# Optimization experiments

Measured on AMD Instinct MI355X. Metric: run time of the kernel, lower is better.

Reference implementation:

```python
import jax, jax.numpy as jnp
import numpy as np
from jax import lax

K = 16        # patch_size / kernel_size
S = 16        # stride
EMB = 768     # embed_dim
CIN = 3


def setup_inputs() -> dict:
    key = jax.random.key(0)
    k1, k2, k3, k4, k5 = jax.random.split(key, 5)
    B, H, W = 64, 384, 384
    pixel_values = jax.random.normal(k1, (B, CIN, H, W), jnp.float32)
    # offset conv: Conv2d(3, 2*K*K, kernel=K, stride=K); small init so offsets stay moderate
    offset_w = jax.random.normal(k2, (2 * K * K, CIN, K, K), jnp.float32) * 0.01
    offset_b = jax.random.normal(k3, (2 * K * K,), jnp.float32) * 0.01
    # deformable projection: DeformConv2d(3, 768, kernel=K, stride=K)
    proj_w = jax.random.normal(k4, (EMB, CIN, K, K), jnp.float32) * 0.02
    proj_b = jax.random.normal(k5, (EMB,), jnp.float32) * 0.02
    return {"pixel_values": pixel_values, "offset_w": offset_w, "offset_b": offset_b,
            "proj_w": proj_w, "proj_b": proj_b}


def _bilinear_gather(img, py, px):
    """img: [B,C,H,W]; py,px: [B,K,K,HO,WO] float sample coords.
    Returns [B,C,K,K,HO,WO] with zero padding outside the image (torchvision semantics)."""
    B, C, H, W = img.shape
    shp = py.shape
    y0 = jnp.floor(py); x0 = jnp.floor(px)
    wy1 = py - y0; wy0 = 1.0 - wy1
    wx1 = px - x0; wx0 = 1.0 - wx1
    imgf = img.reshape(B, C, H * W)

    def corner(yy, xx, w):
        valid = (yy >= 0) & (yy < H) & (xx >= 0) & (xx < W)
        yi = jnp.clip(yy, 0, H - 1).astype(jnp.int32)
        xi = jnp.clip(xx, 0, W - 1).astype(jnp.int32)
        idx = (yi * W + xi).reshape(B, -1)                       # [B, N]
        v = jnp.take_along_axis(imgf, idx[:, None, :], axis=2)   # [B, C, N]
        return v * (jnp.where(valid, w, 0.0)).reshape(B, 1, -1)

    val = (corner(y0, x0, wy0 * wx0) + corner(y0, x0 + 1, wy0 * wx1)
           + corner(y0 + 1, x0, wy1 * wx0) + corner(y0 + 1, x0 + 1, wy1 * wx1))
    return val.reshape((B, C) + shp[1:])


def reference(pixel_values, offset_w, offset_b, proj_w, proj_b):
    B, C, H, W = pixel_values.shape
    HO, WO = H // S, W // S
    # offset conv (dense, stride=patch, VALID padding)
    offset = lax.conv_general_dilated(pixel_values, offset_w, (S, S), 'VALID',
                                      dimension_numbers=('NCHW', 'OIHW', 'NCHW'))
    offset = offset + offset_b[None, :, None, None]              # [B, 2*K*K, HO, WO]
    off = offset.reshape(B, K * K, 2, HO, WO)
    dy = off[:, :, 0].reshape(B, K, K, HO, WO)
    dx = off[:, :, 1].reshape(B, K, K, HO, WO)
    # base sampling grid: p = (ho*S + i + dy, wo*S + j + dx)
    base_y = (jnp.arange(HO, dtype=jnp.float32) * S)[None, None, None, :, None] \
             + jnp.arange(K, dtype=jnp.float32)[None, :, None, None, None]
    base_x = (jnp.arange(WO, dtype=jnp.float32) * S)[None, None, None, None, :] \
             + jnp.arange(K, dtype=jnp.float32)[None, None, :, None, None]
    py = base_y + dy
    px = base_x + dx
    sampled = _bilinear_gather(pixel_values, py, px)             # [B, C, K, K, HO, WO]
    out = jnp.einsum('bcijhw,ocij->bohw', sampled, proj_w) + proj_b[None, :, None, None]
    # flatten(2).transpose(1,2) -> [B, HO*WO, EMB]
    return out.reshape(B, EMB, HO * WO).transpose(0, 2, 1)
```

## Files before the change

kernel.cpp:

```cpp
#include <hip/hip_runtime.h>
#include <stdint.h>

typedef __bf16 bf16x8 __attribute__((ext_vector_type(8)));
typedef float  f32x4  __attribute__((ext_vector_type(4)));

#define HH 384
#define WW 384
#define NPIX (HH*WW)
#define NC 3
#define NPATCH 576
#define EMB 768
#define PLEN 768
#define MLOC 32
#define KSTEPS 24
#define NLOC (64*576)
#define NTILES (NLOC/MLOC)
#define NT1 4
#define W1_UNITS (32*KSTEPS*64)
#define W2_UNITS (48*KSTEPS*64)
#define W2_OFF   (W1_UNITS*8)
#define SA_OFF   ((W1_UNITS+W2_UNITS)*8)
#define WBLKS  ((W1_UNITS + W2_UNITS) / 256)

__device__ __forceinline__ uint16_t f2bf(float f) {
    uint32_t u = __builtin_bit_cast(uint32_t, f);
    u += 0x7FFFu + ((u >> 16) & 1u);
    return (uint16_t)(u >> 16);
}
__device__ __forceinline__ uint32_t pk2(float a, float b) {
    return (uint32_t)f2bf(a) | ((uint32_t)f2bf(b) << 16);
}
__device__ __forceinline__ float bf2f(uint16_t u) {
    return __builtin_bit_cast(float, (uint32_t)u << 16);
}

__global__ __launch_bounds__(256)
void prepass_w(const float* __restrict__ offw, const float* __restrict__ projw,
               uint16_t* __restrict__ wz) {
    int u = blockIdx.x * 256 + threadIdx.x;
    const float* src;
    int uu;
    if (u < W1_UNITS) { src = offw; uu = u; }
    else              { src = projw; uu = u - W1_UNITS; }
    int lane = uu & 63;
    int t    = uu >> 6;
    int ks   = t % KSTEPS;
    int nt   = t / KSTEPS;
    int n    = nt * 16 + (lane & 15);
    int k0   = ks * 32 + (lane >> 4) * 8;
    const float4* s4 = (const float4*)(src + (size_t)n * PLEN + k0);
    float4 v0 = s4[0], v1 = s4[1];
    uint4 w;
    w.x = pk2(v0.x, v0.y); w.y = pk2(v0.z, v0.w);
    w.z = pk2(v1.x, v1.y); w.w = pk2(v1.z, v1.w);
    *(uint4*)(wz + (size_t)u * 8) = w;
}

__global__ __launch_bounds__(512, 4)
void k1_offsets(const float* __restrict__ pix,
                const float* __restrict__ offb,
                const uint16_t* __restrict__ wz,
                uint16_t* __restrict__ sa) {
    __shared__ __align__(16) uint16_t As[MLOC][PLEN];

    const int tid  = threadIdx.x;
    const int wv   = tid >> 6;
    const int lane = tid & 63;
    const int lr   = lane & 15;
    const int lg   = lane >> 4;
    const int sw0  = (lr & 7) << 3;
    const int even = ((lane & 1) == 0);

    int bid = (int)blockIdx.x;
    const int tile = (bid & 7) * 144 + (bid >> 3);
    const int loc0 = tile * MLOC;
    const int bimg = loc0 / NPATCH;
    const int p0   = loc0 - bimg * NPATCH;
    const float* __restrict__ pb = pix + (size_t)bimg * NC * NPIX;

    #pragma unroll
    for (int uu = 0; uu < 6; ++uu) {
        int unit = tid + uu * 512;
        int loc  = unit / 96;
        int k8   = (unit - loc * 96) * 8;
        int c  = k8 >> 8;
        int i  = (k8 >> 4) & 15;
        int j  = k8 & 15;
        int p  = p0 + loc;
        int ho = p / 24;
        int wo = p - ho * 24;
        const float* g = pb + ((size_t)c * HH + ho * 16 + i) * WW + wo * 16 + j;
        float4 v0 = *(const float4*)g;
        float4 v1 = *(const float4*)(g + 4);
        uint4 w;
        w.x = pk2(v0.x, v0.y); w.y = pk2(v0.z, v0.w);
        w.z = pk2(v1.x, v1.y); w.w = pk2(v1.z, v1.w);
        *(uint4*)&As[loc][k8 ^ ((loc & 7) << 3)] = w;
    }

    auto ldb1 = [&](int ntg, int ks) -> bf16x8 {
        return *(const bf16x8*)(wz + ((size_t)((ntg * KSTEPS + ks) * 64 + lane)) * 8);
    };
    bf16x8 b1a[NT1], b1b[NT1];
    #pragma unroll
    for (int nt = 0; nt < NT1; ++nt) b1a[nt] = ldb1(wv * NT1 + nt, 0);
    __syncthreads();

    f32x4 acc1[2][NT1];
    #pragma unroll
    for (int nt = 0; nt < NT1; ++nt) {
        float bz = offb[(wv * NT1 + nt) * 16 + lr];
        f32x4 z = {bz, bz, bz, bz};
        acc1[0][nt] = z; acc1[1][nt] = z;
    }
    #pragma unroll 1
    for (int ks2 = 0; ks2 < KSTEPS / 2; ++ks2) {
        const int ks0 = ks2 * 2;
        {
            #pragma unroll
            for (int nt = 0; nt < NT1; ++nt) b1b[nt] = ldb1(wv * NT1 + nt, ks0 + 1);
            int ke = (ks0 * 32 + lg * 8) ^ sw0;
            bf16x8 a0 = *(const bf16x8*)&As[lr][ke];
            bf16x8 a1 = *(const bf16x8*)&As[16 + lr][ke];
            #pragma unroll
            for (int nt = 0; nt < NT1; ++nt) {
                acc1[0][nt] = __builtin_amdgcn_mfma_f32_16x16x32_bf16(a0, b1a[nt], acc1[0][nt], 0, 0, 0);
                acc1[1][nt] = __builtin_amdgcn_mfma_f32_16x16x32_bf16(a1, b1a[nt], acc1[1][nt], 0, 0, 0);
            }
        }
        {
            int ksn = (ks0 + 2 < KSTEPS) ? ks0 + 2 : 0;
            #pragma unroll
            for (int nt = 0; nt < NT1; ++nt) b1a[nt] = ldb1(wv * NT1 + nt, ksn);
            int ke = ((ks0 + 1) * 32 + lg * 8) ^ sw0;
            bf16x8 a0 = *(const bf16x8*)&As[lr][ke];
            bf16x8 a1 = *(const bf16x8*)&As[16 + lr][ke];
            #pragma unroll
            for (int nt = 0; nt < NT1; ++nt) {
                acc1[0][nt] = __builtin_amdgcn_mfma_f32_16x16x32_bf16(a0, b1b[nt], acc1[0][nt], 0, 0, 0);
                acc1[1][nt] = __builtin_amdgcn_mfma_f32_16x16x32_bf16(a1, b1b[nt], acc1[1][nt], 0, 0, 0);
            }
        }
    }

    #pragma unroll
    for (int nt = 0; nt < NT1; ++nt)
      #pragma unroll
      for (int mt = 0; mt < 2; ++mt)
        #pragma unroll
        for (int r = 0; r < 4; ++r) {
            float v  = acc1[mt][nt][r];
            float pv = __shfl_xor(v, 1);
            if ((nt < 2) == (even != 0)) {
                int s   = nt & 1;
                int loc = mt * 16 + lg * 4 + r;
                int q   = (wv * NT1 + (even ? 0 : 2) + s) * 8 + (lr >> 1);
                float dy = even ? v  : pv;
                float dx = even ? pv : v;
                ((uint32_t*)(sa + (size_t)(loc0 + loc) * PLEN))[q] = pk2(dy, dx);
            }
        }
}

__global__ __launch_bounds__(512)
void k2_gather(const float* __restrict__ pix, uint16_t* __restrict__ sa) {
    const int tid  = threadIdx.x;
    const int wv   = tid >> 6;
    const int lane = tid & 63;

    int bid = (int)blockIdx.x;
    const int tile = (bid & 7) * 144 + (bid >> 3);
    const int loc0 = tile * MLOC;
    const int bimg = loc0 / NPATCH;
    const int p0   = loc0 - bimg * NPATCH;
    const float* __restrict__ pb = pix + (size_t)bimg * NC * NPIX;

    #pragma unroll
    for (int li = 0; li < 4; ++li) {
        const int L   = wv * 4 + li;
        const int p   = p0 + L;
        const int ho  = p / 24;
        const int wo  = p - ho * 24;
        const int by  = ho * 16;
        const int bx  = wo * 16;
        uint16_t* row = sa + (size_t)(loc0 + L) * PLEN;
        const uint32_t* rowu = (const uint32_t*)row;
        uint32_t od0 = rowu[       lane];
        uint32_t od1 = rowu[ 64 +  lane];
        uint32_t od2 = rowu[128 +  lane];
        uint32_t od3 = rowu[192 +  lane];
        asm volatile("s_waitcnt vmcnt(0)" ::: "memory");
        #pragma unroll
        for (int s4 = 0; s4 < 4; ++s4) {
            const int q  = s4 * 64 + lane;
            const int qi = q >> 4;
            const int qj = q & 15;
            uint32_t od = (s4 == 0) ? od0 : (s4 == 1) ? od1 : (s4 == 2) ? od2 : od3;
            float dy = bf2f((uint16_t)od);
            float dx = bf2f((uint16_t)(od >> 16));
            float py = (float)(by + qi) + dy;
            float px = (float)(bx + qj) + dx;
            float y0f = floorf(py), x0f = floorf(px);
            float wy1 = py - y0f, wy0 = 1.f - wy1;
            float wx1 = px - x0f, wx0 = 1.f - wx1;
            int y0 = (int)y0f, x0 = (int)x0f;
            float s0 = 0.f, s1 = 0.f, s2 = 0.f;
            #pragma unroll
            for (int cy = 0; cy < 2; ++cy) {
                int yy = y0 + cy;
                if ((unsigned)yy < (unsigned)HH) {
                    float wy = cy ? wy1 : wy0;
                    #pragma unroll
                    for (int cx = 0; cx < 2; ++cx) {
                        int xx = x0 + cx;
                        if ((unsigned)xx < (unsigned)WW) {
                            float w = wy * (cx ? wx1 : wx0);
                            const float* cp = pb + yy * WW + xx;
                            s0 += w * cp[0];
                            s1 += w * cp[NPIX];
                            s2 += w * cp[2 * NPIX];
                        }
                    }
                }
            }
            row[      q] = f2bf(s0);
            row[256 + q] = f2bf(s1);
            row[512 + q] = f2bf(s2);
        }
    }
}

__global__ __launch_bounds__(256, 3)
void k3_proj(const uint16_t* __restrict__ wz, const float* __restrict__ projb,
             float* __restrict__ out) {
    __shared__ __align__(16) uint16_t Asb[2][128][64];

    const int tid  = threadIdx.x;
    const int wv   = tid >> 6;
    const int lane = tid & 63;
    const int lr   = lane & 15;
    const int lg   = lane >> 4;
    const int wm   = wv >> 1;
    const int wn   = wv & 1;

    int bid = (int)blockIdx.x;
    const int fin   = (bid & 7) * 216 + (bid >> 3);
    const int mtile = fin / 6;
    const int ncol  = fin - mtile * 6;
    const int loc0  = mtile * 128;
    const int n0    = ncol * 128;
    const uint16_t* __restrict__ sa = wz + SA_OFF;

    const int srow = tid >> 1;
    const int shalf = tid & 1;
    const int srb = srow & 7;
    const uint16_t* sg = sa + (size_t)(loc0 + srow) * PLEN + shalf * 32;

    uint4 r0, r1, r2, r3;
    auto st_load = [&](int t) {
        const uint16_t* g = sg + t * 64;
        r0 = *(const uint4*)g;
        r1 = *(const uint4*)(g + 8);
        r2 = *(const uint4*)(g + 16);
        r3 = *(const uint4*)(g + 24);
    };
    auto st_write = [&](int buf) {
        uint16_t* dst = &Asb[buf][srow][0];
        *(uint4*)(dst + (((shalf * 4 + 0) ^ srb) * 8)) = r0;
        *(uint4*)(dst + (((shalf * 4 + 1) ^ srb) * 8)) = r1;
        *(uint4*)(dst + (((shalf * 4 + 2) ^ srb) * 8)) = r2;
        *(uint4*)(dst + (((shalf * 4 + 3) ^ srb) * 8)) = r3;
    };
    auto ldb = [&](int nt, int ks) -> bf16x8 {
        int ntg = ncol * 8 + wn * 4 + nt;
        return *(const bf16x8*)(wz + W2_OFF + ((size_t)((ntg * KSTEPS + ks) * 64 + lane)) * 8);
    };

    f32x4 acc[4][4];
    #pragma unroll
    for (int nt = 0; nt < 4; ++nt) {
        float bz = projb[n0 + wn * 64 + nt * 16 + lr];
        f32x4 z = {bz, bz, bz, bz};
        #pragma unroll
        for (int mi = 0; mi < 4; ++mi) acc[mi][nt] = z;
    }

    bf16x8 ba[4], bb[4];
    st_load(0);
    st_write(0);
    #pragma unroll
    for (int nt = 0; nt < 4; ++nt) ba[nt] = ldb(nt, 0);
    __syncthreads();

    #pragma unroll 1
    for (int t = 0; t < 12; ++t) {
        const int cur = t & 1;
        if (t < 11) st_load(t + 1);
        {
            #pragma unroll
            for (int nt = 0; nt < 4; ++nt) bb[nt] = ldb(nt, t * 2 + 1);
            bf16x8 a0, a1, a2, a3;
            {
                const int u = ((0 * 4 + lg) ^ (lr & 7)) * 8;
                a0 = *(const bf16x8*)&Asb[cur][wm * 64 +  0 + lr][u];
                a1 = *(const bf16x8*)&Asb[cur][wm * 64 + 16 + lr][u];
                a2 = *(const bf16x8*)&Asb[cur][wm * 64 + 32 + lr][u];
                a3 = *(const bf16x8*)&Asb[cur][wm * 64 + 48 + lr][u];
            }
            #pragma unroll
            for (int nt = 0; nt < 4; ++nt) {
                acc[0][nt] = __builtin_amdgcn_mfma_f32_16x16x32_bf16(a0, ba[nt], acc[0][nt], 0, 0, 0);
                acc[1][nt] = __builtin_amdgcn_mfma_f32_16x16x32_bf16(a1, ba[nt], acc[1][nt], 0, 0, 0);
                acc[2][nt] = __builtin_amdgcn_mfma_f32_16x16x32_bf16(a2, ba[nt], acc[2][nt], 0, 0, 0);
                acc[3][nt] = __builtin_amdgcn_mfma_f32_16x16x32_bf16(a3, ba[nt], acc[3][nt], 0, 0, 0);
            }
        }
        {
            if (t < 11) {
                #pragma unroll
                for (int nt = 0; nt < 4; ++nt) ba[nt] = ldb(nt, t * 2 + 2);
            }
            bf16x8 a0, a1, a2, a3;
            {
                const int u = ((1 * 4 + lg) ^ (lr & 7)) * 8;
                a0 = *(const bf16x8*)&Asb[cur][wm * 64 +  0 + lr][u];
                a1 = *(const bf16x8*)&Asb[cur][wm * 64 + 16 + lr][u];
                a2 = *(const bf16x8*)&Asb[cur][wm * 64 + 32 + lr][u];
                a3 = *(const bf16x8*)&Asb[cur][wm * 64 + 48 + lr][u];
            }
            #pragma unroll
            for (int nt = 0; nt < 4; ++nt) {
                acc[0][nt] = __builtin_amdgcn_mfma_f32_16x16x32_bf16(a0, bb[nt], acc[0][nt], 0, 0, 0);
                acc[1][nt] = __builtin_amdgcn_mfma_f32_16x16x32_bf16(a1, bb[nt], acc[1][nt], 0, 0, 0);
                acc[2][nt] = __builtin_amdgcn_mfma_f32_16x16x32_bf16(a2, bb[nt], acc[2][nt], 0, 0, 0);
                acc[3][nt] = __builtin_amdgcn_mfma_f32_16x16x32_bf16(a3, bb[nt], acc[3][nt], 0, 0, 0);
            }
        }
        if (t < 11) st_write(cur ^ 1);
        __syncthreads();
    }

    #pragma unroll
    for (int mi = 0; mi < 4; ++mi)
      #pragma unroll
      for (int r = 0; r < 4; ++r) {
        int rowg = loc0 + wm * 64 + mi * 16 + lg * 4 + r;
        float* op = out + (size_t)rowg * EMB + n0 + wn * 64;
        #pragma unroll
        for (int nt = 0; nt < 4; ++nt)
            op[nt * 16 + lr] = acc[mi][nt][r];
      }
}

__global__ __launch_bounds__(256)
void fallback_kernel(const float* __restrict__ pix, const float* __restrict__ offw,
                     const float* __restrict__ offb, const float* __restrict__ projw,
                     const float* __restrict__ projb, float* __restrict__ out) {
    __shared__ float buf[8][PLEN];
    const int tid = threadIdx.x;
    const int loc0 = blockIdx.x * 8;
    #pragma unroll
    for (int r = 0; r < 6; ++r) {
        int item = tid + r * 256;
        int l = item / 192, k = (item - l * 192) * 4;
        int c = k >> 8, i = (k >> 4) & 15, j = k & 15;
        int flat = loc0 + l, b = flat / NPATCH, p = flat - b * NPATCH;
        int ho = p / 24, wo = p - ho * 24;
        *(float4*)(&buf[l][k]) = *(const float4*)(pix +
            (((size_t)b * NC + c) * HH + (size_t)ho * 16 + i) * WW + wo * 16 + j);
    }
    __syncthreads();
    float dy[8], dx[8];
    {
        float a0[8], a1[8];
        float b0 = offb[2 * tid], b1 = offb[2 * tid + 1];
        #pragma unroll
        for (int l = 0; l < 8; ++l) { a0[l] = b0; a1[l] = b1; }
        const float4* w0 = (const float4*)(offw + (size_t)(2 * tid) * PLEN);
        const float4* w1 = w0 + PLEN / 4;
        for (int k4 = 0; k4 < PLEN / 4; ++k4) {
            float4 wa = w0[k4], wb = w1[k4];
            #pragma unroll
            for (int l = 0; l < 8; ++l) {
                float4 pv = *(const float4*)(&buf[l][k4 * 4]);
                a0[l] += wa.x*pv.x + wa.y*pv.y + wa.z*pv.z + wa.w*pv.w;
                a1[l] += wb.x*pv.x + wb.y*pv.y + wb.z*pv.z + wb.w*pv.w;
            }
        }
        #pragma unroll
        for (int l = 0; l < 8; ++l) { dy[l] = a0[l]; dx[l] = a1[l]; }
    }
    __syncthreads();
    {
        const int i = tid >> 4, j = tid & 15;
        #pragma unroll
        for (int l = 0; l < 8; ++l) {
            int flat = loc0 + l, b = flat / NPATCH, p = flat - b * NPATCH;
            int ho = p / 24, wo = p - ho * 24;
            float py = (float)(ho * 16 + i) + dy[l];
            float px = (float)(wo * 16 + j) + dx[l];
            float y0 = floorf(py), x0 = floorf(px);
            float wy1 = py - y0, wy0 = 1.f - wy1, wx1 = px - x0, wx0 = 1.f - wx1;
            const float* pb = pix + (size_t)b * NC * NPIX;
            float s0 = 0, s1 = 0, s2 = 0;
            #pragma unroll
            for (int cy = 0; cy < 2; ++cy)
              #pragma unroll
              for (int cx = 0; cx < 2; ++cx) {
                int yy = (int)y0 + cy, xx = (int)x0 + cx;
                float w = (cy ? wy1 : wy0) * (cx ? wx1 : wx0);
                if ((unsigned)yy < (unsigned)HH && (unsigned)xx < (unsigned)WW) {
                    int idx = yy * WW + xx;
                    s0 += w * pb[idx]; s1 += w * pb[NPIX + idx]; s2 += w * pb[2*NPIX + idx];
                }
              }
            buf[l][tid] = s0; buf[l][256 + tid] = s1; buf[l][512 + tid] = s2;
        }
    }
    __syncthreads();
    {
        float aA[8], aB[8], aC[8];
        float bA = projb[tid], bB = projb[tid + 256], bC = projb[tid + 512];
        #pragma unroll
        for (int l = 0; l < 8; ++l) { aA[l] = bA; aB[l] = bB; aC[l] = bC; }
        const float4* wA = (const float4*)(projw + (size_t)tid * PLEN);
        const float4* wB = (const float4*)(projw + (size_t)(tid + 256) * PLEN);
        const float4* wC = (const float4*)(projw + (size_t)(tid + 512) * PLEN);
        for (int k4 = 0; k4 < PLEN / 4; ++k4) {
            float4 a = wA[k4], bq = wB[k4], cq = wC[k4];
            #pragma unroll
            for (int l = 0; l < 8; ++l) {
                float4 pv = *(const float4*)(&buf[l][k4 * 4]);
                aA[l] += a.x*pv.x + a.y*pv.y + a.z*pv.z + a.w*pv.w;
                aB[l] += bq.x*pv.x + bq.y*pv.y + bq.z*pv.z + bq.w*pv.w;
                aC[l] += cq.x*pv.x + cq.y*pv.y + cq.z*pv.z + cq.w*pv.w;
            }
        }
        #pragma unroll
        for (int l = 0; l < 8; ++l) {
            float* op = out + (size_t)(loc0 + l) * EMB;
            op[tid] = aA[l]; op[tid + 256] = aB[l]; op[tid + 512] = aC[l];
        }
    }
}

extern "C" void kernel_launch(void* const* d_in, const int* in_sizes, int n_in,
                              void* d_out, int out_size, void* d_ws, size_t ws_size,
                              hipStream_t stream) {
    const float* pix   = (const float*)d_in[0];
    const float* offw  = (const float*)d_in[1];
    const float* offb  = (const float*)d_in[2];
    const float* projw = (const float*)d_in[3];
    const float* projb = (const float*)d_in[4];
    float* out = (float*)d_out;
    uint16_t* wz = (uint16_t*)d_ws;

    const size_t ws_needed = (size_t)SA_OFF * 2 + (size_t)NLOC * PLEN * 2;

    if (ws_size >= ws_needed) {
        uint16_t* sa = wz + SA_OFF;
        prepass_w<<<WBLKS, 256, 0, stream>>>(offw, projw, wz);
        k1_offsets<<<NTILES, 512, 0, stream>>>(pix, offb, wz, sa);
        k2_gather<<<NTILES, 512, 0, stream>>>(pix, sa);
        k3_proj<<<288 * 6, 256, 0, stream>>>(wz, projb, out);
    } else {
        fallback_kernel<<<NLOC / 8, 256, 0, stream>>>(pix, offw, offb, projw, projb, out);
    }
}
```

Before: 215.6 us.

## Pre-im2col patches to bf16 and retile offset GEMM with async LDS loads

The prepass now also converts pixel bands to bf16 and writes an im2col patch matrix into the workspace. The offset conv becomes a 128x128-tiled GEMM over that matrix, using direct global-to-LDS loads with swizzle, replacing the old 32-row tiles that each loaded the full weight panel. The projection GEMM also switches its A staging from register round-trips to global_load_lds. This trades an extra write and read of a large bf16 patch buffer for better weight reuse and fewer register-staged copies.

```diff
diff --git a/kernel.cpp b/kernel.cpp
--- a/kernel.cpp
+++ b/kernel.cpp
@@ -11,16 +11,15 @@
 #define NPATCH 576
 #define EMB 768
 #define PLEN 768
-#define MLOC 32
 #define KSTEPS 24
 #define NLOC (64*576)
-#define NTILES (NLOC/MLOC)
-#define NT1 4
 #define W1_UNITS (32*KSTEPS*64)
 #define W2_UNITS (48*KSTEPS*64)
 #define W2_OFF   (W1_UNITS*8)
-#define SA_OFF   ((W1_UNITS+W2_UNITS)*8)
-#define WBLKS  ((W1_UNITS + W2_UNITS) / 256)
+#define AP_OFF   ((W1_UNITS+W2_UNITS)*8)
+#define SA_OFF   (AP_OFF + NLOC*PLEN)
+#define P0_WBLKS ((W1_UNITS+W2_UNITS)/256)
+#define P0_BANDS (64*24)
 
 __device__ __forceinline__ uint16_t f2bf(float f) {
     uint32_t u = __builtin_bit_cast(uint32_t, f);
@@ -35,129 +34,163 @@
 }
 
 __global__ __launch_bounds__(256)
-void prepass_w(const float* __restrict__ offw, const float* __restrict__ projw,
-               uint16_t* __restrict__ wz) {
-    int u = blockIdx.x * 256 + threadIdx.x;
-    const float* src;
-    int uu;
-    if (u < W1_UNITS) { src = offw; uu = u; }
-    else              { src = projw; uu = u - W1_UNITS; }
-    int lane = uu & 63;
-    int t    = uu >> 6;
-    int ks   = t % KSTEPS;
-    int nt   = t / KSTEPS;
-    int n    = nt * 16 + (lane & 15);
-    int k0   = ks * 32 + (lane >> 4) * 8;
-    const float4* s4 = (const float4*)(src + (size_t)n * PLEN + k0);
-    float4 v0 = s4[0], v1 = s4[1];
-    uint4 w;
-    w.x = pk2(v0.x, v0.y); w.y = pk2(v0.z, v0.w);
-    w.z = pk2(v1.x, v1.y); w.w = pk2(v1.z, v1.w);
-    *(uint4*)(wz + (size_t)u * 8) = w;
-}
-
-__global__ __launch_bounds__(512, 4)
-void k1_offsets(const float* __restrict__ pix,
-                const float* __restrict__ offb,
-                const uint16_t* __restrict__ wz,
-                uint16_t* __restrict__ sa) {
-    __shared__ __align__(16) uint16_t As[MLOC][PLEN];
-
-    const int tid  = threadIdx.x;
-    const int wv   = tid >> 6;
-    const int lane = tid & 63;
-    const int lr   = lane & 15;
-    const int lg   = lane >> 4;
-    const int sw0  = (lr & 7) << 3;
-    const int even = ((lane & 1) == 0);
-
-    int bid = (int)blockIdx.x;
-    const int tile = (bid & 7) * 144 + (bid >> 3);
-    const int loc0 = tile * MLOC;
-    const int bimg = loc0 / NPATCH;
-    const int p0   = loc0 - bimg * NPATCH;
-    const float* __restrict__ pb = pix + (size_t)bimg * NC * NPIX;
-
-    #pragma unroll
-    for (int uu = 0; uu < 6; ++uu) {
-        int unit = tid + uu * 512;
-        int loc  = unit / 96;
-        int k8   = (unit - loc * 96) * 8;
-        int c  = k8 >> 8;
-        int i  = (k8 >> 4) & 15;
-        int j  = k8 & 15;
-        int p  = p0 + loc;
-        int ho = p / 24;
-        int wo = p - ho * 24;
-        const float* g = pb + ((size_t)c * HH + ho * 16 + i) * WW + wo * 16 + j;
-        float4 v0 = *(const float4*)g;
-        float4 v1 = *(const float4*)(g + 4);
+void p0_prepass(const float* __restrict__ offw, const float* __restrict__ projw,
+                const float* __restrict__ pix, uint16_t* __restrict__ wz) {
+    __shared__ uint16_t L[3 * 16 * 384];
+    int b = blockIdx.x;
+    if (b < P0_WBLKS) {
+        int u = b * 256 + threadIdx.x;
+        const float* src;
+        int uu;
+        if (u < W1_UNITS) { src = offw; uu = u; }
+        else              { src = projw; uu = u - W1_UNITS; }
+        int lane = uu & 63;
+        int t    = uu >> 6;
+        int ks   = t % KSTEPS;
+        int nt   = t / KSTEPS;
+        int n    = nt * 16 + (lane & 15);
+        int k0   = ks * 32 + (lane >> 4) * 8;
+        const float4* s4 = (const float4*)(src + (size_t)n * PLEN + k0);
+        float4 v0 = s4[0], v1 = s4[1];
         uint4 w;
         w.x = pk2(v0.x, v0.y); w.y = pk2(v0.z, v0.w);
         w.z = pk2(v1.x, v1.y); w.w = pk2(v1.z, v1.w);
-        *(uint4*)&As[loc][k8 ^ ((loc & 7) << 3)] = w;
-    }
-
-    auto ldb1 = [&](int ntg, int ks) -> bf16x8 {
+        *(uint4*)(wz + (size_t)u * 8) = w;
+        return;
+    }
+    int band = b - P0_WBLKS;
+    int img  = band / 24;
+    int yb   = band - img * 24;
+    const float* src = pix + (size_t)img * NC * NPIX + (size_t)yb * 16 * WW;
+    #pragma unroll
+    for (int i = 0; i < 18; ++i) {
+        int u = threadIdx.x + i * 256;
+        int c = u / 1536;
+        int r = u - c * 1536;
+        float4 v = *(const float4*)(src + (size_t)c * NPIX + (size_t)r * 4);
+        uint2 o;
+        o.x = pk2(v.x, v.y);
+        o.y = pk2(v.z, v.w);
+        *(uint2*)&L[c * 6144 + r * 4] = o;
+    }
+    __syncthreads();
+    uint16_t* ap = wz + AP_OFF + (size_t)(img * NPATCH + yb * 24) * PLEN;
+    #pragma unroll
+    for (int i = 0; i < 9; ++i) {
+        int u  = threadIdx.x + i * 256;
+        int p  = u / 96;
+        int k8 = (u - p * 96) * 8;
+        int c  = k8 >> 8;
+        int ii = (k8 >> 4) & 15;
+        int j  = k8 & 15;
+        uint4 d = *(const uint4*)&L[(c * 16 + ii) * 384 + p * 16 + j];
+        *(uint4*)(ap + (size_t)p * PLEN + k8) = d;
+    }
+}
+
+__global__ __launch_bounds__(256, 3)
+void k1_offgemm(const uint16_t* __restrict__ wz, const float* __restrict__ offb,
+                uint16_t* __restrict__ sa) {
+    __shared__ __align__(16) uint16_t Asb[2][128][64];
+    const int tid = threadIdx.x, wv = tid >> 6, lane = tid & 63;
+    const int lr = lane & 15, lg = lane >> 4;
+    const int wm = wv >> 1, wn = wv & 1;
+    int bid = (int)blockIdx.x;
+    const int fin   = (bid & 7) * 144 + (bid >> 3);
+    const int mtile = fin >> 2;
+    const int nc    = fin & 3;
+    const int loc0  = mtile * 128;
+    const int n0    = nc * 128;
+    const uint16_t* __restrict__ Ap = wz + AP_OFF;
+
+    const uint16_t* gs[4];
+    #pragma unroll
+    for (int l = 0; l < 4; ++l) {
+        int u = l * 256 + tid;
+        int row = u >> 3, ch = u & 7;
+        gs[l] = Ap + (size_t)(loc0 + row) * PLEN + (ch ^ (row & 7)) * 8;
+    }
+    auto stage = [&](int t, int buf) {
+        #pragma unroll
+        for (int l = 0; l < 4; ++l)
+            __builtin_amdgcn_global_load_lds(
+                (const uint32_t*)(gs[l] + t * 64),
+                (uint32_t*)((uint16_t*)&Asb[buf][0][0] + (size_t)(l * 256 + wv * 64) * 8),
+                16, 0, 0);
+    };
+    auto ldb = [&](int nt, int ks) -> bf16x8 {
+        int ntg = nc * 8 + wn * 4 + nt;
         return *(const bf16x8*)(wz + ((size_t)((ntg * KSTEPS + ks) * 64 + lane)) * 8);
     };
-    bf16x8 b1a[NT1], b1b[NT1];
-    #pragma unroll
-    for (int nt = 0; nt < NT1; ++nt) b1a[nt] = ldb1(wv * NT1 + nt, 0);
-    __syncthreads();
-
-    f32x4 acc1[2][NT1];
-    #pragma unroll
-    for (int nt = 0; nt < NT1; ++nt) {
-        float bz = offb[(wv * NT1 + nt) * 16 + lr];
+
+    f32x4 acc[4][4];
+    #pragma unroll
+    for (int nt = 0; nt < 4; ++nt) {
+        float bz = offb[n0 + wn * 64 + nt * 16 + lr];
         f32x4 z = {bz, bz, bz, bz};
-        acc1[0][nt] = z; acc1[1][nt] = z;
-    }
+        #pragma unroll
+        for (int mi = 0; mi < 4; ++mi) acc[mi][nt] = z;
+    }
+
+    bf16x8 ba[4], bb[4];
+    stage(0, 0);
+    #pragma unroll
+    for (int nt = 0; nt < 4; ++nt) ba[nt] = ldb(nt, 0);
+    __syncthreads();
+
     #pragma unroll 1
-    for (int ks2 = 0; ks2 < KSTEPS / 2; ++ks2) {
-        const int ks0 = ks2 * 2;
+    for (int t = 0; t < 12; ++t) {
+        const int cur = t & 1;
+        if (t < 11) stage(t + 1, cur ^ 1);
         {
             #pragma unroll
-            for (int nt = 0; nt < NT1; ++nt) b1b[nt] = ldb1(wv * NT1 + nt, ks0 + 1);
-            int ke = (ks0 * 32 + lg * 8) ^ sw0;
-            bf16x8 a0 = *(const bf16x8*)&As[lr][ke];
-            bf16x8 a1 = *(const bf16x8*)&As[16 + lr][ke];
-            #pragma unroll
-            for (int nt = 0; nt < NT1; ++nt) {
-                acc1[0][nt] = __builtin_amdgcn_mfma_f32_16x16x32_bf16(a0, b1a[nt], acc1[0][nt], 0, 0, 0);
-                acc1[1][nt] = __builtin_amdgcn_mfma_f32_16x16x32_bf16(a1, b1a[nt], acc1[1][nt], 0, 0, 0);
+            for (int nt = 0; nt < 4; ++nt) bb[nt] = ldb(nt, 2 * t + 1);
+            const int u0 = (lg ^ (lr & 7)) * 8;
+            bf16x8 a0 = *(const bf16x8*)&Asb[cur][wm * 64 +  0 + lr][u0];
+            bf16x8 a1 = *(const bf16x8*)&Asb[cur][wm * 64 + 16 + lr][u0];
+            bf16x8 a2 = *(const bf16x8*)&Asb[cur][wm * 64 + 32 + lr][u0];
+            bf16x8 a3 = *(const bf16x8*)&Asb[cur][wm * 64 + 48 + lr][u0];
+            #pragma unroll
+            for (int nt = 0; nt < 4; ++nt) {
+                acc[0][nt] = __builtin_amdgcn_mfma_f32_16x16x32_bf16(a0, ba[nt], acc[0][nt], 0, 0, 0);
+                acc[1][nt] = __builtin_amdgcn_mfma_f32_16x16x32_bf16(a1, ba[nt], acc[1][nt], 0, 0, 0);
+                acc[2][nt] = __builtin_amdgcn_mfma_f32_16x16x32_bf16(a2, ba[nt], acc[2][nt], 0, 0, 0);
+                acc[3][nt] = __builtin_amdgcn_mfma_f32_16x16x32_bf16(a3, ba[nt], acc[3][nt], 0, 0, 0);
             }
         }
         {
-            int ksn = (ks0 + 2 < KSTEPS) ? ks0 + 2 : 0;
-            #pragma unroll
-            for (int nt = 0; nt < NT1; ++nt) b1a[nt] = ldb1(wv * NT1 + nt, ksn);
-            int ke = ((ks0 + 1) * 32 + lg * 8) ^ sw0;
-            bf16x8 a0 = *(const bf16x8*)&As[lr][ke];
-            bf16x8 a1 = *(const bf16x8*)&As[16 + lr][ke];
-            #pragma unroll
-            for (int nt = 0; nt < NT1; ++nt) {
-                acc1[0][nt] = __builtin_amdgcn_mfma_f32_16x16x32_bf16(a0, b1b[nt], acc1[0][nt], 0, 0, 0);
-                acc1[1][nt] = __builtin_amdgcn_mfma_f32_16x16x32_bf16(a1, b1b[nt], acc1[1][nt], 0, 0, 0);
-            }
-        }
-    }
-
-    #pragma unroll
-    for (int nt = 0; nt < NT1; ++nt)
+            if (t < 11) {
+                #pragma unroll
+                for (int nt = 0; nt < 4; ++nt) ba[nt] = ldb(nt, 2 * t + 2);
+            }
+            const int u1 = ((4 + lg) ^ (lr & 7)) * 8;
+            bf16x8 a0 = *(const bf16x8*)&Asb[cur][wm * 64 +  0 + lr][u1];
+            bf16x8 a1 = *(const bf16x8*)&Asb[cur][wm * 64 + 16 + lr][u1];
+            bf16x8 a2 = *(const bf16x8*)&Asb[cur][wm * 64 + 32 + lr][u1];
+            bf16x8 a3 = *(const bf16x8*)&Asb[cur][wm * 64 + 48 + lr][u1];
+            #pragma unroll
+            for (int nt = 0; nt < 4; ++nt) {
+                acc[0][nt] = __builtin_amdgcn_mfma_f32_16x16x32_bf16(a0, bb[nt], acc[0][nt], 0, 0, 0);
+                acc[1][nt] = __builtin_amdgcn_mfma_f32_16x16x32_bf16(a1, bb[nt], acc[1][nt], 0, 0, 0);
+                acc[2][nt] = __builtin_amdgcn_mfma_f32_16x16x32_bf16(a2, bb[nt], acc[2][nt], 0, 0, 0);
+                acc[3][nt] = __builtin_amdgcn_mfma_f32_16x16x32_bf16(a3, bb[nt], acc[3][nt], 0, 0, 0);
+            }
+        }
+        __syncthreads();
+    }
+
+    #pragma unroll
+    for (int nt = 0; nt < 4; ++nt)
       #pragma unroll
-      for (int mt = 0; mt < 2; ++mt)
+      for (int mi = 0; mi < 4; ++mi)
         #pragma unroll
         for (int r = 0; r < 4; ++r) {
-            float v  = acc1[mt][nt][r];
+            float v  = acc[mi][nt][r];
             float pv = __shfl_xor(v, 1);
-            if ((nt < 2) == (even != 0)) {
-                int s   = nt & 1;
-                int loc = mt * 16 + lg * 4 + r;
-                int q   = (wv * NT1 + (even ? 0 : 2) + s) * 8 + (lr >> 1);
-                float dy = even ? v  : pv;
-                float dx = even ? pv : v;
-                ((uint32_t*)(sa + (size_t)(loc0 + loc) * PLEN))[q] = pk2(dy, dx);
+            if ((lane & 1) == 0) {
+                int row = loc0 + wm * 64 + mi * 16 + lg * 4 + r;
+                int q   = (n0 >> 1) + wn * 32 + nt * 8 + (lr >> 1);
+                ((uint32_t*)(sa + (size_t)row * PLEN))[q] = pk2(v, pv);
             }
         }
 }
@@ -167,10 +200,9 @@
     const int tid  = threadIdx.x;
     const int wv   = tid >> 6;
     const int lane = tid & 63;
-
     int bid = (int)blockIdx.x;
     const int tile = (bid & 7) * 144 + (bid >> 3);
-    const int loc0 = tile * MLOC;
+    const int loc0 = tile * 32;
     const int bimg = loc0 / NPATCH;
     const int p0   = loc0 - bimg * NPATCH;
     const float* __restrict__ pb = pix + (size_t)bimg * NC * NPIX;
@@ -234,15 +266,9 @@
 void k3_proj(const uint16_t* __restrict__ wz, const float* __restrict__ projb,
              float* __restrict__ out) {
     __shared__ __align__(16) uint16_t Asb[2][128][64];
-
-    const int tid  = threadIdx.x;
-    const int wv   = tid >> 6;
-    const int lane = tid & 63;
-    const int lr   = lane & 15;
-    const int lg   = lane >> 4;
-    const int wm   = wv >> 1;
-    const int wn   = wv & 1;
-
+    const int tid = threadIdx.x, wv = tid >> 6, lane = tid & 63;
+    const int lr = lane & 15, lg = lane >> 4;
+    const int wm = wv >> 1, wn = wv & 1;
     int bid = (int)blockIdx.x;
     const int fin   = (bid & 7) * 216 + (bid >> 3);
     const int mtile = fin / 6;
@@ -251,25 +277,20 @@
     const int n0    = ncol * 128;
     const uint16_t* __restrict__ sa = wz + SA_OFF;
 
-    const int srow = tid >> 1;
-    const int shalf = tid & 1;
-    const int srb = srow & 7;
-    const uint16_t* sg = sa + (size_t)(loc0 + srow) * PLEN + shalf * 32;
-
-    uint4 r0, r1, r2, r3;
-    auto st_load = [&](int t) {
-        const uint16_t* g = sg + t * 64;
-        r0 = *(const uint4*)g;
-        r1 = *(const uint4*)(g + 8);
-        r2 = *(const uint4*)(g + 16);
-        r3 = *(const uint4*)(g + 24);
-    };
-    auto st_write = [&](int buf) {
-        uint16_t* dst = &Asb[buf][srow][0];
-        *(uint4*)(dst + (((shalf * 4 + 0) ^ srb) * 8)) = r0;
-        *(uint4*)(dst + (((shalf * 4 + 1) ^ srb) * 8)) = r1;
-        *(uint4*)(dst + (((shalf * 4 + 2) ^ srb) * 8)) = r2;
-        *(uint4*)(dst + (((shalf * 4 + 3) ^ srb) * 8)) = r3;
+    const uint16_t* gs[4];
+    #pragma unroll
+    for (int l = 0; l < 4; ++l) {
+        int u = l * 256 + tid;
+        int row = u >> 3, ch = u & 7;
+        gs[l] = sa + (size_t)(loc0 + row) * PLEN + (ch ^ (row & 7)) * 8;
+    }
+    auto stage = [&](int t, int buf) {
+        #pragma unroll
+        for (int l = 0; l < 4; ++l)
+            __builtin_amdgcn_global_load_lds(
+                (const uint32_t*)(gs[l] + t * 64),
+                (uint32_t*)((uint16_t*)&Asb[buf][0][0] + (size_t)(l * 256 + wv * 64) * 8),
+                16, 0, 0);
     };
     auto ldb = [&](int nt, int ks) -> bf16x8 {
         int ntg = ncol * 8 + wn * 4 + nt;
@@ -286,8 +307,7 @@
     }
 
     bf16x8 ba[4], bb[4];
-    st_load(0);
-    st_write(0);
+    stage(0, 0);
     #pragma unroll
     for (int nt = 0; nt < 4; ++nt) ba[nt] = ldb(nt, 0);
     __syncthreads();
@@ -295,18 +315,15 @@
     #pragma unroll 1
     for (int t = 0; t < 12; ++t) {
         const int cur = t & 1;
-        if (t < 11) st_load(t + 1);
+        if (t < 11) stage(t + 1, cur ^ 1);
         {
             #pragma unroll
-            for (int nt = 0; nt < 4; ++nt) bb[nt] = ldb(nt, t * 2 + 1);
-            bf16x8 a0, a1, a2, a3;
-            {
-                const int u = ((0 * 4 + lg) ^ (lr & 7)) * 8;
-                a0 = *(const bf16x8*)&Asb[cur][wm * 64 +  0 + lr][u];
-                a1 = *(const bf16x8*)&Asb[cur][wm * 64 + 16 + lr][u];
-                a2 = *(const bf16x8*)&Asb[cur][wm * 64 + 32 + lr][u];
-                a3 = *(const bf16x8*)&Asb[cur][wm * 64 + 48 + lr][u];
-            }
+            for (int nt = 0; nt < 4; ++nt) bb[nt] = ldb(nt, 2 * t + 1);
+            const int u0 = (lg ^ (lr & 7)) * 8;
+            bf16x8 a0 = *(const bf16x8*)&Asb[cur][wm * 64 +  0 + lr][u0];
+            bf16x8 a1 = *(const bf16x8*)&Asb[cur][wm * 64 + 16 + lr][u0];
+            bf16x8 a2 = *(const bf16x8*)&Asb[cur][wm * 64 + 32 + lr][u0];
+            bf16x8 a3 = *(const bf16x8*)&Asb[cur][wm * 64 + 48 + lr][u0];
             #pragma unroll
             for (int nt = 0; nt < 4; ++nt) {
                 acc[0][nt] = __builtin_amdgcn_mfma_f32_16x16x32_bf16(a0, ba[nt], acc[0][nt], 0, 0, 0);
@@ -318,16 +335,13 @@
         {
             if (t < 11) {
                 #pragma unroll
-                for (int nt = 0; nt < 4; ++nt) ba[nt] = ldb(nt, t * 2 + 2);
-            }
-            bf16x8 a0, a1, a2, a3;
-            {
-                const int u = ((1 * 4 + lg) ^ (lr & 7)) * 8;
-                a0 = *(const bf16x8*)&Asb[cur][wm * 64 +  0 + lr][u];
-                a1 = *(const bf16x8*)&Asb[cur][wm * 64 + 16 + lr][u];
-                a2 = *(const bf16x8*)&Asb[cur][wm * 64 + 32 + lr][u];
-                a3 = *(const bf16x8*)&Asb[cur][wm * 64 + 48 + lr][u];
-            }
+                for (int nt = 0; nt < 4; ++nt) ba[nt] = ldb(nt, 2 * t + 2);
+            }
+            const int u1 = ((4 + lg) ^ (lr & 7)) * 8;
+            bf16x8 a0 = *(const bf16x8*)&Asb[cur][wm * 64 +  0 + lr][u1];
+            bf16x8 a1 = *(const bf16x8*)&Asb[cur][wm * 64 + 16 + lr][u1];
+            bf16x8 a2 = *(const bf16x8*)&Asb[cur][wm * 64 + 32 + lr][u1];
+            bf16x8 a3 = *(const bf16x8*)&Asb[cur][wm * 64 + 48 + lr][u1];
             #pragma unroll
             for (int nt = 0; nt < 4; ++nt) {
                 acc[0][nt] = __builtin_amdgcn_mfma_f32_16x16x32_bf16(a0, bb[nt], acc[0][nt], 0, 0, 0);
@@ -336,7 +350,6 @@
                 acc[3][nt] = __builtin_amdgcn_mfma_f32_16x16x32_bf16(a3, bb[nt], acc[3][nt], 0, 0, 0);
             }
         }
-        if (t < 11) st_write(cur ^ 1);
         __syncthreads();
     }
 
@@ -455,14 +468,14 @@
     float* out = (float*)d_out;
     uint16_t* wz = (uint16_t*)d_ws;
 
-    const size_t ws_needed = (size_t)SA_OFF * 2 + (size_t)NLOC * PLEN * 2;
+    const size_t ws_needed = ((size_t)SA_OFF + (size_t)NLOC * PLEN) * 2;
 
     if (ws_size >= ws_needed) {
         uint16_t* sa = wz + SA_OFF;
-        prepass_w<<<WBLKS, 256, 0, stream>>>(offw, projw, wz);
-        k1_offsets<<<NTILES, 512, 0, stream>>>(pix, offb, wz, sa);
-        k2_gather<<<NTILES, 512, 0, stream>>>(pix, sa);
-        k3_proj<<<288 * 6, 256, 0, stream>>>(wz, projb, out);
+        p0_prepass<<<P0_WBLKS + P0_BANDS, 256, 0, stream>>>(offw, projw, pix, wz);
+        k1_offgemm<<<1152, 256, 0, stream>>>(wz, offb, sa);
+        k2_gather<<<1152, 512, 0, stream>>>(pix, sa);
+        k3_proj<<<1728, 256, 0, stream>>>(wz, projb, out);
     } else {
         fallback_kernel<<<NLOC / 8, 256, 0, stream>>>(pix, offw, offb, projw, projb, out);
     }
```

Measured after the change: 217.3 us. About the same (+0.8%).
